# Kernel optimization log

Hardware: AMD Instinct MI355X
Metric: run time of the kernel (lower is better)

## Reference

```python
import jax, jax.numpy as jnp
import numpy as np

H = 64  # hidden_dim

def _lstm_dir(x, Wih, Whh, bih, bhh, reverse):
    # x: [B, T, D]; Wih: [4H, D]; Whh: [4H, H]; PyTorch gate order i,f,g,o
    B, T, _ = x.shape
    if reverse:
        x = x[:, ::-1, :]
    # Precompute input contribution to all gates: [B, T, 4H]
    xg = jnp.einsum('btd,gd->btg', x, Wih) + (bih + bhh)
    h0 = jnp.zeros((B, H), x.dtype)
    c0 = jnp.zeros((B, H), x.dtype)

    def step(carry, xg_t):
        h, c = carry
        g = xg_t + h @ Whh.T  # [B, 4H]
        i, f, gg, o = jnp.split(g, 4, axis=-1)
        i = jax.nn.sigmoid(i)
        f = jax.nn.sigmoid(f)
        gg = jnp.tanh(gg)
        o = jax.nn.sigmoid(o)
        c = f * c + i * gg
        h = o * jnp.tanh(c)
        return (h, c), h

    (hT, cT), hs = jax.lax.scan(step, (h0, c0), jnp.swapaxes(xg, 0, 1))
    hs = jnp.swapaxes(hs, 0, 1)  # [B, T, H]
    if reverse:
        hs = hs[:, ::-1, :]
    return hs, hT

def _forward(x, Wih_l0_f, Whh_l0_f, bih_l0_f, bhh_l0_f,
             Wih_l0_b, Whh_l0_b, bih_l0_b, bhh_l0_b,
             Wih_l1_f, Whh_l1_f, bih_l1_f, bhh_l1_f,
             Wih_l1_b, Whh_l1_b, bih_l1_b, bhh_l1_b,
             fc1_W, fc1_b, fc2_W, fc2_b):
    xt = jnp.transpose(x, (0, 2, 1))  # [B, 512, 3]
    # Layer 0 (bidirectional)
    hs_f, _ = _lstm_dir(xt, Wih_l0_f, Whh_l0_f, bih_l0_f, bhh_l0_f, False)
    hs_b, _ = _lstm_dir(xt, Wih_l0_b, Whh_l0_b, bih_l0_b, bhh_l0_b, True)
    y0 = jnp.concatenate([hs_f, hs_b], axis=-1)  # [B, 512, 2H]
    # (inter-layer dropout is identity in eval mode)
    # Layer 1 (bidirectional); only final hidden states needed
    _, hT_f = _lstm_dir(y0, Wih_l1_f, Whh_l1_f, bih_l1_f, bhh_l1_f, False)
    _, hT_b = _lstm_dir(y0, Wih_l1_b, Whh_l1_b, bih_l1_b, bhh_l1_b, True)
    h = jnp.concatenate([hT_f, hT_b], axis=-1)  # [B, 2H]
    h = jax.nn.relu(h @ fc1_W.T + fc1_b)
    return h @ fc2_W.T + fc2_b  # [B, num_classes]

def setup_inputs() -> dict:
    key = jax.random.key(0)
    ks = iter(jax.random.split(key, 32))
    B, T, C = 1024, 512, 3
    d = {}
    d['x'] = jax.random.normal(next(ks), (B, C, T), dtype=jnp.float32)
    # PyTorch-style bias init: forget-gate bias = 1, rest 0
    bias = jnp.zeros((4 * H,), jnp.float32).at[H:2 * H].set(1.0)
    for layer, din in [(0, C), (1, 2 * H)]:
        for dirn in ['f', 'b']:
            d[f'Wih_l{layer}_{dirn}'] = jax.random.normal(next(ks), (4 * H, din), dtype=jnp.float32) * 0.1
            d[f'Whh_l{layer}_{dirn}'] = jax.random.normal(next(ks), (4 * H, H), dtype=jnp.float32) * 0.1
            d[f'bih_l{layer}_{dirn}'] = bias
            d[f'bhh_l{layer}_{dirn}'] = jnp.zeros((4 * H,), jnp.float32)
    d['fc1_W'] = jax.random.normal(next(ks), (H, 2 * H), dtype=jnp.float32) * 0.1
    d['fc1_b'] = jnp.zeros((H,), jnp.float32)
    d['fc2_W'] = jax.random.normal(next(ks), (2, H), dtype=jnp.float32) * 0.1
    d['fc2_b'] = jnp.zeros((2,), jnp.float32)
    return d

def reference(x, Wih_l0_f, Whh_l0_f, bih_l0_f, bhh_l0_f,
              Wih_l0_b, Whh_l0_b, bih_l0_b, bhh_l0_b,
              Wih_l1_f, Whh_l1_f, bih_l1_f, bhh_l1_f,
              Wih_l1_b, Whh_l1_b, bih_l1_b, bhh_l1_b,
              fc1_W, fc1_b, fc2_W, fc2_b):
    return _forward(x, Wih_l0_f, Whh_l0_f, bih_l0_f, bhh_l0_f,
                    Wih_l0_b, Whh_l0_b, bih_l0_b, bhh_l0_b,
                    Wih_l1_f, Whh_l1_f, bih_l1_f, bhh_l1_f,
                    Wih_l1_b, Whh_l1_b, bih_l1_b, bhh_l1_b,
                    fc1_W, fc1_b, fc2_W, fc2_b)
```

## Files before the change

### kernel.cpp

```cpp
#include <hip/hip_runtime.h>
#include <stdint.h>

typedef __attribute__((ext_vector_type(8))) short short8;
typedef __attribute__((ext_vector_type(4))) float f32x4;

#define TT 512
#define LSTR 136
#define XS 516

static __device__ __forceinline__ uint32_t f2bf_u(float f){
  union { float f; uint32_t u; } v; v.f = f;
  return (v.u + 0x7fffu + ((v.u >> 16) & 1u)) >> 16;
}
static __device__ __forceinline__ short8 w8f32(const float* p){
  float4 a = *(const float4*)p;
  float4 b = *(const float4*)(p + 4);
  short8 r;
  r[0] = (short)f2bf_u(a.x); r[1] = (short)f2bf_u(a.y);
  r[2] = (short)f2bf_u(a.z); r[3] = (short)f2bf_u(a.w);
  r[4] = (short)f2bf_u(b.x); r[5] = (short)f2bf_u(b.y);
  r[6] = (short)f2bf_u(b.z); r[7] = (short)f2bf_u(b.w);
  return r;
}
static __device__ __forceinline__ float sigx(float x){
  float e = __builtin_amdgcn_exp2f(-1.442695040888963f * x);
  return __builtin_amdgcn_rcpf(1.f + e);
}
static __device__ __forceinline__ float tanhx(float x){
  float e = __builtin_amdgcn_exp2f(-2.885390081777927f * x);
  return fmaf(__builtin_amdgcn_rcpf(1.f + e), 2.f, -1.f);
}
static __device__ __forceinline__ void lds_barrier(){
  asm volatile("s_waitcnt lgkmcnt(0)" ::: "memory");
  __builtin_amdgcn_s_barrier();
}
#define MF(A,B,C) __builtin_amdgcn_mfma_f32_16x16x32_bf16((A),(B),(C),0,0,0)

__global__ __launch_bounds__(256, 2) void lstm_l0(
    const float* __restrict__ x,
    const float* __restrict__ Wih_f, const float* __restrict__ Whh_f,
    const float* __restrict__ bih_f, const float* __restrict__ bhh_f,
    const float* __restrict__ Wih_b, const float* __restrict__ Whh_b,
    const float* __restrict__ bih_b, const float* __restrict__ bhh_b,
    unsigned short* __restrict__ y0)
{
  const int tid = threadIdx.x;
  const int wv = tid >> 6, lane = tid & 63;
  const int quad = lane >> 4, m16 = lane & 15;
  const int dir = blockIdx.y;
  const int bbase = blockIdx.x * 4;
  const float* Wih = dir ? Wih_b : Wih_f;
  const float* Whh = dir ? Whh_b : Whh_f;
  const float* bih = dir ? bih_b : bih_f;
  const float* bhh = dir ? bhh_b : bhh_f;

  __shared__ __align__(16) unsigned short sZ[2][4][LSTR];
  __shared__ __align__(16) float sX[12 * XS];

  const int copy = m16 >> 2;
  const int batch = m16 & 3;
  const int unit = 16 * wv + 4 * copy + quad;
  const bool selA = (copy & 1) != 0;
  const bool selB = (copy & 2) != 0;

  short8 aH[4][2];
  const int gm = (m16 & 3) * 64 + (m16 >> 2);
  #pragma unroll
  for (int k = 0; k < 4; k++){
    const int g = gm + 4 * (4 * wv + k);
    aH[k][0] = w8f32(Whh + g * 64 + quad * 8);
    aH[k][1] = w8f32(Whh + g * 64 + 32 + quad * 8);
  }
  float Wf[4][3];
  f32x4 biasF;
  #pragma unroll
  for (int r = 0; r < 4; r++){
    biasF[r] = bih[r * 64 + unit] + bhh[r * 64 + unit];
    #pragma unroll
    for (int d = 0; d < 3; d++) Wf[r][d] = Wih[(r * 64 + unit) * 3 + d];
  }

  for (int idx = tid; idx < 2 * 4 * LSTR; idx += 256)
    ((unsigned short*)sZ)[idx] = 0;
  for (int i4 = tid; i4 < 1536; i4 += 256){
    const int row = i4 >> 7, t4 = (i4 & 127) * 4;
    *(float4*)&sX[row * XS + t4] = *(const float4*)(x + (size_t)bbase * 1536 + row * 512 + t4);
  }
  __syncthreads();

  const int xrow = 3 * batch;
  float c = 0.f, h = 0.f;
  const f32x4 z4 = {0.f, 0.f, 0.f, 0.f};

#define FFCOMP(F, TIDX) do { \
    float x0_ = sX[xrow * XS + (TIDX)]; \
    float x1_ = sX[(xrow + 1) * XS + (TIDX)]; \
    float x2_ = sX[(xrow + 2) * XS + (TIDX)]; \
    _Pragma("unroll") \
    for (int r_ = 0; r_ < 4; r_++) \
      F[r_] = fmaf(Wf[r_][2], x2_, fmaf(Wf[r_][1], x1_, fmaf(Wf[r_][0], x0_, biasF[r_]))); \
  } while(0)

  f32x4 FBa, FBb;
  {
    const int t0_ = dir ? (TT - 1) : 0;
    FFCOMP(FBa, t0_);
  }

#define L0STEP(S, P, FC, FN) do { \
    const int p1_ = (P) ^ 1; \
    short8 bh0 = *(const short8*)&sZ[P][batch][     quad * 8]; \
    short8 bh1 = *(const short8*)&sZ[P][batch][32 + quad * 8]; \
    if (wv == 3 && lane < 32 && (S) > 0){ \
      const int tprev = dir ? (TT - (S)) : ((S) - 1); \
      const int br_ = lane >> 3, cc_ = lane & 7; \
      uint4 v_ = *(const uint4*)&sZ[P][br_][cc_ * 8]; \
      *(uint4*)(y0 + ((size_t)(bbase + br_) * TT + tprev) * 128 + dir * 64 + cc_ * 8) = v_; \
    } \
    f32x4 C0 = MF(aH[0][0], bh0, z4); \
    f32x4 C1 = MF(aH[1][0], bh0, z4); \
    f32x4 C2 = MF(aH[2][0], bh0, z4); \
    f32x4 C3 = MF(aH[3][0], bh0, z4); \
    C0 = MF(aH[0][1], bh1, C0); \
    C1 = MF(aH[1][1], bh1, C1); \
    C2 = MF(aH[2][1], bh1, C2); \
    C3 = MF(aH[3][1], bh1, C3); \
    { int sn_ = (S) + 1; if (sn_ > TT - 1) sn_ = TT - 1; \
      const int tn_ = dir ? (TT - 1 - sn_) : sn_; \
      FFCOMP(FN, tn_); \
    } \
    __builtin_amdgcn_sched_barrier(0); \
    { \
      float g0_ = (selB ? (selA ? C3[0] : C2[0]) : (selA ? C1[0] : C0[0])) + FC[0]; \
      float g1_ = (selB ? (selA ? C3[1] : C2[1]) : (selA ? C1[1] : C0[1])) + FC[1]; \
      float g2_ = (selB ? (selA ? C3[2] : C2[2]) : (selA ? C1[2] : C0[2])) + FC[2]; \
      float g3_ = (selB ? (selA ? C3[3] : C2[3]) : (selA ? C1[3] : C0[3])) + FC[3]; \
      float ii_ = sigx(g0_), ff_ = sigx(g1_), gg_ = tanhx(g2_), oo_ = sigx(g3_); \
      c = fmaf(ff_, c, ii_ * gg_); \
      h = oo_ * tanhx(c); \
      sZ[p1_][batch][unit] = (unsigned short)f2bf_u(h); \
    } \
    __builtin_amdgcn_sched_barrier(0); \
    lds_barrier(); \
  } while(0)

  for (int s = 0; s < TT; s += 2){
    L0STEP(s,     0, FBa, FBb);
    L0STEP(s + 1, 1, FBb, FBa);
  }
#undef L0STEP
#undef FFCOMP

  if (wv == 3 && lane < 32){
    const int tl = dir ? 0 : (TT - 1);
    const int br = lane >> 3, cc = lane & 7;
    uint4 v = *(const uint4*)&sZ[0][br][cc * 8];
    *(uint4*)(y0 + ((size_t)(bbase + br) * TT + tl) * 128 + dir * 64 + cc * 8) = v;
  }
}

#define NONLIN_WRITE(A0V, A1V, P1) do { \
    float g0_ = sel0 ? (A0V)[0] : (A1V)[0]; \
    float g1_ = sel0 ? (A0V)[1] : (A1V)[1]; \
    float g2_ = sel0 ? (A0V)[2] : (A1V)[2]; \
    float g3_ = sel0 ? (A0V)[3] : (A1V)[3]; \
    float ii_ = sigx(g0_), ff_ = sigx(g1_), gg_ = tanhx(g2_), oo_ = sigx(g3_); \
    c = fmaf(ff_, c, ii_ * gg_); \
    h = oo_ * tanhx(c); \
    sZ[P1][m8][colw] = (unsigned short)f2bf_u(h); \
  } while(0)

__global__ __launch_bounds__(512, 2) void lstm_l1(
    const unsigned short* __restrict__ y0,
    const float* __restrict__ Wih_f, const float* __restrict__ Whh_f,
    const float* __restrict__ bih_f, const float* __restrict__ bhh_f,
    const float* __restrict__ Wih_b, const float* __restrict__ Whh_b,
    const float* __restrict__ bih_b, const float* __restrict__ bhh_b,
    float* __restrict__ hT)
{
  const int tid = threadIdx.x;
  const int wv = tid >> 6, lane = tid & 63;
  const int quad = lane >> 4, m16 = lane & 15;
  const int dir = blockIdx.y;
  const int bbase = blockIdx.x * 8;
  const float* Wih = dir ? Wih_b : Wih_f;
  const float* Whh = dir ? Whh_b : Whh_f;
  const float* bih = dir ? bih_b : bih_f;
  const float* bhh = dir ? bhh_b : bhh_f;

  __shared__ __align__(16) unsigned short sZ[2][8][LSTR];
  __shared__ __align__(16) unsigned short sY[4][8][LSTR];

  short8 aY[2][4], aH[2][2];
  f32x4 biasv[2];
  const int gm = (m16 & 3) * 64 + (m16 >> 2);
  #pragma unroll
  for (int i = 0; i < 2; i++){
    const int rt = 2 * wv + i;
    const int g = gm + 4 * rt;
    #pragma unroll
    for (int kt = 0; kt < 4; kt++) aY[i][kt] = w8f32(Wih + g * 128 + kt * 32 + quad * 8);
    aH[i][0] = w8f32(Whh + g * 64 + quad * 8);
    aH[i][1] = w8f32(Whh + g * 64 + 32 + quad * 8);
    const int gu = 4 * rt + quad;
    #pragma unroll
    for (int r = 0; r < 4; r++) biasv[i][r] = bih[r * 64 + gu] + bhh[r * 64 + gu];
  }

  for (int idx = tid; idx < 2 * 8 * LSTR; idx += 512)
    ((unsigned short*)sZ)[idx] = 0;

  const bool stager = (lane < 16);
  const size_t sgbase = (size_t)(bbase + wv) * TT * 128 + (size_t)lane * 8;
  float4 hA = make_float4(0.f,0.f,0.f,0.f), hB = make_float4(0.f,0.f,0.f,0.f);
  if (stager){
    const int t0 = dir ? (TT-1) : 0, t1 = dir ? (TT-2) : 1, t2 = dir ? (TT-3) : 2;
    const int t3 = dir ? (TT-4) : 3, t4 = dir ? (TT-5) : 4;
    float4 v0 = *(const float4*)(y0 + sgbase + (size_t)t0 * 128);
    float4 v1 = *(const float4*)(y0 + sgbase + (size_t)t1 * 128);
    float4 v2 = *(const float4*)(y0 + sgbase + (size_t)t2 * 128);
    hA = *(const float4*)(y0 + sgbase + (size_t)t3 * 128);
    hB = *(const float4*)(y0 + sgbase + (size_t)t4 * 128);
    *(float4*)&sY[0][wv][lane * 8] = v0;
    *(float4*)&sY[1][wv][lane * 8] = v1;
    *(float4*)&sY[2][wv][lane * 8] = v2;
  }
  __syncthreads();

  const int m8 = m16 & 7;
  const bool sel0 = (m16 < 8);
  const int colw = 8 * wv + quad + ((m16 >> 3) << 2);
  float c = 0.f, h = 0.f;

  f32x4 FBa0, FBa1, FBb0, FBb1;
  {
    short8 by0 = *(const short8*)&sY[0][m8][     quad * 8];
    short8 by1 = *(const short8*)&sY[0][m8][32 + quad * 8];
    short8 by2 = *(const short8*)&sY[0][m8][64 + quad * 8];
    short8 by3 = *(const short8*)&sY[0][m8][96 + quad * 8];
    FBa0 = MF(aY[0][0], by0, biasv[0]);
    FBa1 = MF(aY[1][0], by0, biasv[1]);
    FBa0 = MF(aY[0][1], by1, FBa0);  FBa1 = MF(aY[1][1], by1, FBa1);
    FBa0 = MF(aY[0][2], by2, FBa0);  FBa1 = MF(aY[1][2], by2, FBa1);
    FBa0 = MF(aY[0][3], by3, FBa0);  FBa1 = MF(aY[1][3], by3, FBa1);
  }

#define L1STEP(S, P, SLOT, WSLOT, HOLD, FC0, FC1, FN0, FN1) do { \
    const int p1_ = (P) ^ 1; \
    short8 bh0 = *(const short8*)&sZ[P][m8][     quad * 8]; \
    short8 bh1 = *(const short8*)&sZ[P][m8][32 + quad * 8]; \
    short8 by0 = *(const short8*)&sY[SLOT][m8][     quad * 8]; \
    short8 by1 = *(const short8*)&sY[SLOT][m8][32 + quad * 8]; \
    short8 by2 = *(const short8*)&sY[SLOT][m8][64 + quad * 8]; \
    short8 by3 = *(const short8*)&sY[SLOT][m8][96 + quad * 8]; \
    f32x4 A0 = MF(aH[0][0], bh0, FC0); \
    f32x4 A1 = MF(aH[1][0], bh0, FC1); \
    A0 = MF(aH[0][1], bh1, A0); \
    A1 = MF(aH[1][1], bh1, A1); \
    FN0 = MF(aY[0][0], by0, biasv[0]); \
    FN1 = MF(aY[1][0], by0, biasv[1]); \
    FN0 = MF(aY[0][1], by1, FN0);  FN1 = MF(aY[1][1], by1, FN1); \
    FN0 = MF(aY[0][2], by2, FN0);  FN1 = MF(aY[1][2], by2, FN1); \
    FN0 = MF(aY[0][3], by3, FN0);  FN1 = MF(aY[1][3], by3, FN1); \
    __builtin_amdgcn_sched_barrier(0); \
    NONLIN_WRITE(A0, A1, p1_); \
    if ((S) == TT - 1){ \
      hT[(size_t)(bbase + m8) * 128 + dir * 64 + colw] = h; \
    } \
    if (stager){ \
      *(float4*)&sY[WSLOT][wv][lane * 8] = HOLD; \
      int sg_ = (S) + 5; if (sg_ > TT - 1) sg_ = TT - 1; \
      const int tg_ = dir ? (TT - 1 - sg_) : sg_; \
      HOLD = *(const float4*)(y0 + sgbase + (size_t)tg_ * 128); \
    } \
    __builtin_amdgcn_sched_barrier(0); \
    lds_barrier(); \
  } while(0)

  for (int s = 0; s < TT; s += 4){
    L1STEP(s,     0, 1, 3, hA, FBa0, FBa1, FBb0, FBb1);
    L1STEP(s + 1, 1, 2, 0, hB, FBb0, FBb1, FBa0, FBa1);
    L1STEP(s + 2, 0, 3, 1, hA, FBa0, FBa1, FBb0, FBb1);
    L1STEP(s + 3, 1, 0, 2, hB, FBb0, FBb1, FBa0, FBa1);
  }
#undef L1STEP
}

__global__ __launch_bounds__(256, 1) void fc_kernel(
    const float* __restrict__ hT,
    const float* __restrict__ w1, const float* __restrict__ b1,
    const float* __restrict__ w2, const float* __restrict__ b2,
    float* __restrict__ out)
{
  __shared__ float sh[4][64];
  const int wave = threadIdx.x >> 6, lane = threadIdx.x & 63;
  const int b = blockIdx.x * 4 + wave;
  float acc = b1[lane];
  const float* hrow = hT + (size_t)b * 128;
  #pragma unroll
  for (int k = 0; k < 128; k += 4){
    float4 h4 = *(const float4*)(hrow + k);
    float4 w4 = *(const float4*)(w1 + lane * 128 + k);
    acc = fmaf(w4.x, h4.x, acc);
    acc = fmaf(w4.y, h4.y, acc);
    acc = fmaf(w4.z, h4.z, acc);
    acc = fmaf(w4.w, h4.w, acc);
  }
  sh[wave][lane] = fmaxf(acc, 0.f);
  __syncthreads();
  if (lane < 2){
    float a = b2[lane];
    #pragma unroll
    for (int k = 0; k < 64; k++) a = fmaf(w2[lane * 64 + k], sh[wave][k], a);
    out[(size_t)b * 2 + lane] = a;
  }
}

extern "C" void kernel_launch(void* const* d_in, const int* in_sizes, int n_in,
                              void* d_out, int out_size, void* d_ws, size_t ws_size,
                              hipStream_t stream){
  (void)in_sizes; (void)n_in; (void)out_size; (void)ws_size;
  const float* x     = (const float*)d_in[0];
  const float* Wih0f = (const float*)d_in[1];
  const float* Whh0f = (const float*)d_in[2];
  const float* bih0f = (const float*)d_in[3];
  const float* bhh0f = (const float*)d_in[4];
  const float* Wih0b = (const float*)d_in[5];
  const float* Whh0b = (const float*)d_in[6];
  const float* bih0b = (const float*)d_in[7];
  const float* bhh0b = (const float*)d_in[8];
  const float* Wih1f = (const float*)d_in[9];
  const float* Whh1f = (const float*)d_in[10];
  const float* bih1f = (const float*)d_in[11];
  const float* bhh1f = (const float*)d_in[12];
  const float* Wih1b = (const float*)d_in[13];
  const float* Whh1b = (const float*)d_in[14];
  const float* bih1b = (const float*)d_in[15];
  const float* bhh1b = (const float*)d_in[16];
  const float* fc1W  = (const float*)d_in[17];
  const float* fc1b  = (const float*)d_in[18];
  const float* fc2W  = (const float*)d_in[19];
  const float* fc2b  = (const float*)d_in[20];
  float* out = (float*)d_out;

  unsigned short* y0 = (unsigned short*)d_ws;
  float* hT = (float*)((char*)d_ws + (size_t)1024 * TT * 128 * 2);

  lstm_l0<<<dim3(256, 2), dim3(256), 0, stream>>>(x, Wih0f, Whh0f, bih0f, bhh0f,
                                                  Wih0b, Whh0b, bih0b, bhh0b, y0);
  lstm_l1<<<dim3(128, 2), dim3(512), 0, stream>>>(y0, Wih1f, Whh1f, bih1f, bhh1f,
                                                  Wih1b, Whh1b, bih1b, bhh1b, hT);
  fc_kernel<<<dim3(256), dim3(256), 0, stream>>>(hT, fc1W, fc1b, fc2W, fc2b, out);
}
```

Baseline: 517.1 us.

## Compute layer-1 input projection for two timesteps per MFMA batch using both half-lanes

The layer-1 kernel previously spent 8 MFMAs every step on the input projection, half of whose output lanes were discarded by the select. It now loads two consecutive timesteps' inputs into the two 8-row halves of the B operand. One 8-MFMA batch therefore yields the projections for two steps, and a ds_swizzle exchanges values between half-lanes to route each step's gates to the right lanes. The recurrent MFMAs now start from zero and the precomputed gate input is added before the nonlinearities. The staging prefetch distance grows by one slot. This halves input-projection MFMA work per step, at the cost of extra swizzles, register pressure and an alternating A/B step structure.

```diff
diff --git a/kernel.cpp b/kernel.cpp
--- a/kernel.cpp
+++ b/kernel.cpp
@@ -35,6 +35,7 @@
   __builtin_amdgcn_s_barrier();
 }
 #define MF(A,B,C) __builtin_amdgcn_mfma_f32_16x16x32_bf16((A),(B),(C),0,0,0)
+#define SWZ(x) __int_as_float(__builtin_amdgcn_ds_swizzle(__float_as_int(x), 0x201F))
 
 __global__ __launch_bounds__(256, 2) void lstm_l0(
     const float* __restrict__ x,
@@ -159,17 +160,6 @@
   }
 }
 
-#define NONLIN_WRITE(A0V, A1V, P1) do { \
-    float g0_ = sel0 ? (A0V)[0] : (A1V)[0]; \
-    float g1_ = sel0 ? (A0V)[1] : (A1V)[1]; \
-    float g2_ = sel0 ? (A0V)[2] : (A1V)[2]; \
-    float g3_ = sel0 ? (A0V)[3] : (A1V)[3]; \
-    float ii_ = sigx(g0_), ff_ = sigx(g1_), gg_ = tanhx(g2_), oo_ = sigx(g3_); \
-    c = fmaf(ff_, c, ii_ * gg_); \
-    h = oo_ * tanhx(c); \
-    sZ[P1][m8][colw] = (unsigned short)f2bf_u(h); \
-  } while(0)
-
 __global__ __launch_bounds__(512, 2) void lstm_l1(
     const unsigned short* __restrict__ y0,
     const float* __restrict__ Wih_f, const float* __restrict__ Whh_f,
@@ -214,16 +204,14 @@
   const size_t sgbase = (size_t)(bbase + wv) * TT * 128 + (size_t)lane * 8;
   float4 hA = make_float4(0.f,0.f,0.f,0.f), hB = make_float4(0.f,0.f,0.f,0.f);
   if (stager){
-    const int t0 = dir ? (TT-1) : 0, t1 = dir ? (TT-2) : 1, t2 = dir ? (TT-3) : 2;
-    const int t3 = dir ? (TT-4) : 3, t4 = dir ? (TT-5) : 4;
-    float4 v0 = *(const float4*)(y0 + sgbase + (size_t)t0 * 128);
-    float4 v1 = *(const float4*)(y0 + sgbase + (size_t)t1 * 128);
-    float4 v2 = *(const float4*)(y0 + sgbase + (size_t)t2 * 128);
-    hA = *(const float4*)(y0 + sgbase + (size_t)t3 * 128);
-    hB = *(const float4*)(y0 + sgbase + (size_t)t4 * 128);
-    *(float4*)&sY[0][wv][lane * 8] = v0;
-    *(float4*)&sY[1][wv][lane * 8] = v1;
-    *(float4*)&sY[2][wv][lane * 8] = v2;
+    #pragma unroll
+    for (int k = 0; k < 4; k++){
+      const int tk = dir ? (TT - 1 - k) : k;
+      *(float4*)&sY[k][wv][lane * 8] = *(const float4*)(y0 + sgbase + (size_t)tk * 128);
+    }
+    const int t4 = dir ? (TT - 5) : 4, t5 = dir ? (TT - 6) : 5;
+    hA = *(const float4*)(y0 + sgbase + (size_t)t4 * 128);
+    hB = *(const float4*)(y0 + sgbase + (size_t)t5 * 128);
   }
   __syncthreads();
 
@@ -231,59 +219,102 @@
   const bool sel0 = (m16 < 8);
   const int colw = 8 * wv + quad + ((m16 >> 3) << 2);
   float c = 0.f, h = 0.f;
-
-  f32x4 FBa0, FBa1, FBb0, FBb1;
-  {
-    short8 by0 = *(const short8*)&sY[0][m8][     quad * 8];
-    short8 by1 = *(const short8*)&sY[0][m8][32 + quad * 8];
-    short8 by2 = *(const short8*)&sY[0][m8][64 + quad * 8];
-    short8 by3 = *(const short8*)&sY[0][m8][96 + quad * 8];
-    FBa0 = MF(aY[0][0], by0, biasv[0]);
-    FBa1 = MF(aY[1][0], by0, biasv[1]);
-    FBa0 = MF(aY[0][1], by1, FBa0);  FBa1 = MF(aY[1][1], by1, FBa1);
-    FBa0 = MF(aY[0][2], by2, FBa0);  FBa1 = MF(aY[1][2], by2, FBa1);
-    FBa0 = MF(aY[0][3], by3, FBa0);  FBa1 = MF(aY[1][3], by3, FBa1);
-  }
-
-#define L1STEP(S, P, SLOT, WSLOT, HOLD, FC0, FC1, FN0, FN1) do { \
-    const int p1_ = (P) ^ 1; \
-    short8 bh0 = *(const short8*)&sZ[P][m8][     quad * 8]; \
-    short8 bh1 = *(const short8*)&sZ[P][m8][32 + quad * 8]; \
-    short8 by0 = *(const short8*)&sY[SLOT][m8][     quad * 8]; \
-    short8 by1 = *(const short8*)&sY[SLOT][m8][32 + quad * 8]; \
-    short8 by2 = *(const short8*)&sY[SLOT][m8][64 + quad * 8]; \
-    short8 by3 = *(const short8*)&sY[SLOT][m8][96 + quad * 8]; \
-    f32x4 A0 = MF(aH[0][0], bh0, FC0); \
-    f32x4 A1 = MF(aH[1][0], bh0, FC1); \
-    A0 = MF(aH[0][1], bh1, A0); \
-    A1 = MF(aH[1][1], bh1, A1); \
-    FN0 = MF(aY[0][0], by0, biasv[0]); \
-    FN1 = MF(aY[1][0], by0, biasv[1]); \
-    FN0 = MF(aY[0][1], by1, FN0);  FN1 = MF(aY[1][1], by1, FN1); \
-    FN0 = MF(aY[0][2], by2, FN0);  FN1 = MF(aY[1][2], by2, FN1); \
-    FN0 = MF(aY[0][3], by3, FN0);  FN1 = MF(aY[1][3], by3, FN1); \
-    __builtin_amdgcn_sched_barrier(0); \
-    NONLIN_WRITE(A0, A1, p1_); \
+  const f32x4 z4 = {0.f, 0.f, 0.f, 0.f};
+
+  const int SLOTU = 8 * LSTR;
+  const unsigned short* yb = &sY[0][0][0] + (sel0 ? 0 : SLOTU) + m8 * LSTR + quad * 8;
+
+#define FFMM(SL, FB0, FB1) do { \
+    short8 by0 = *(const short8*)(yb + (SL) * SLOTU); \
+    short8 by1 = *(const short8*)(yb + (SL) * SLOTU + 32); \
+    short8 by2 = *(const short8*)(yb + (SL) * SLOTU + 64); \
+    short8 by3 = *(const short8*)(yb + (SL) * SLOTU + 96); \
+    FB0 = MF(aY[0][0], by0, biasv[0]); \
+    FB1 = MF(aY[1][0], by0, biasv[1]); \
+    FB0 = MF(aY[0][1], by1, FB0);  FB1 = MF(aY[1][1], by1, FB1); \
+    FB0 = MF(aY[0][2], by2, FB0);  FB1 = MF(aY[1][2], by2, FB1); \
+    FB0 = MF(aY[0][3], by3, FB0);  FB1 = MF(aY[1][3], by3, FB1); \
+  } while(0)
+
+#define FFSWZ(FB0, FB1, G0, G1) do { \
+    float w10_ = SWZ(FB1[0]), w11_ = SWZ(FB1[1]), w12_ = SWZ(FB1[2]), w13_ = SWZ(FB1[3]); \
+    float w00_ = SWZ(FB0[0]), w01_ = SWZ(FB0[1]), w02_ = SWZ(FB0[2]), w03_ = SWZ(FB0[3]); \
+    G0[0] = sel0 ? FB0[0] : w10_;  G0[1] = sel0 ? FB0[1] : w11_; \
+    G0[2] = sel0 ? FB0[2] : w12_;  G0[3] = sel0 ? FB0[3] : w13_; \
+    G1[0] = sel0 ? w00_ : FB1[0];  G1[1] = sel0 ? w01_ : FB1[1]; \
+    G1[2] = sel0 ? w02_ : FB1[2];  G1[3] = sel0 ? w03_ : FB1[3]; \
+  } while(0)
+
+  f32x4 Ga0, Ga1, Gb0, Gb1, FBT0, FBT1;
+  FFMM(0, FBT0, FBT1);
+  FFSWZ(FBT0, FBT1, Ga0, Ga1);
+  lds_barrier();
+
+#define NONLIN1(R0, R1, GC, P1) do { \
+    float g0_ = (sel0 ? (R0)[0] : (R1)[0]) + GC[0]; \
+    float g1_ = (sel0 ? (R0)[1] : (R1)[1]) + GC[1]; \
+    float g2_ = (sel0 ? (R0)[2] : (R1)[2]) + GC[2]; \
+    float g3_ = (sel0 ? (R0)[3] : (R1)[3]) + GC[3]; \
+    float ii_ = sigx(g0_), ff_ = sigx(g1_), gg_ = tanhx(g2_), oo_ = sigx(g3_); \
+    c = fmaf(ff_, c, ii_ * gg_); \
+    h = oo_ * tanhx(c); \
+    sZ[P1][m8][colw] = (unsigned short)f2bf_u(h); \
+  } while(0)
+
+#define STAGE(S, WRSL, HOLD) do { \
+    if (stager){ \
+      *(float4*)&sY[WRSL][wv][lane * 8] = HOLD; \
+      int sg_ = (S) + 6; if (sg_ > TT - 1) sg_ = TT - 1; \
+      const int tg_ = dir ? (TT - 1 - sg_) : sg_; \
+      HOLD = *(const float4*)(y0 + sgbase + (size_t)tg_ * 128); \
+    } \
+  } while(0)
+
+#define L1STEPA(S, SLFF, WRSL, HOLD, GC) do { \
+    short8 bh0 = *(const short8*)&sZ[0][m8][     quad * 8]; \
+    short8 bh1 = *(const short8*)&sZ[0][m8][32 + quad * 8]; \
+    f32x4 R0 = MF(aH[0][0], bh0, z4); \
+    f32x4 R1 = MF(aH[1][0], bh0, z4); \
+    R0 = MF(aH[0][1], bh1, R0); \
+    R1 = MF(aH[1][1], bh1, R1); \
+    FFMM(SLFF, FBT0, FBT1); \
+    STAGE(S, WRSL, HOLD); \
+    __builtin_amdgcn_sched_barrier(0); \
+    NONLIN1(R0, R1, GC, 1); \
+    __builtin_amdgcn_sched_barrier(0); \
+    lds_barrier(); \
+  } while(0)
+
+#define L1STEPB(S, WRSL, HOLD, GC, GN0, GN1) do { \
+    short8 bh0 = *(const short8*)&sZ[1][m8][     quad * 8]; \
+    short8 bh1 = *(const short8*)&sZ[1][m8][32 + quad * 8]; \
+    f32x4 R0 = MF(aH[0][0], bh0, z4); \
+    f32x4 R1 = MF(aH[1][0], bh0, z4); \
+    R0 = MF(aH[0][1], bh1, R0); \
+    R1 = MF(aH[1][1], bh1, R1); \
+    FFSWZ(FBT0, FBT1, GN0, GN1); \
+    STAGE(S, WRSL, HOLD); \
+    __builtin_amdgcn_sched_barrier(0); \
+    NONLIN1(R0, R1, GC, 0); \
     if ((S) == TT - 1){ \
       hT[(size_t)(bbase + m8) * 128 + dir * 64 + colw] = h; \
     } \
-    if (stager){ \
-      *(float4*)&sY[WSLOT][wv][lane * 8] = HOLD; \
-      int sg_ = (S) + 5; if (sg_ > TT - 1) sg_ = TT - 1; \
-      const int tg_ = dir ? (TT - 1 - sg_) : sg_; \
-      HOLD = *(const float4*)(y0 + sgbase + (size_t)tg_ * 128); \
-    } \
     __builtin_amdgcn_sched_barrier(0); \
     lds_barrier(); \
   } while(0)
 
   for (int s = 0; s < TT; s += 4){
-    L1STEP(s,     0, 1, 3, hA, FBa0, FBa1, FBb0, FBb1);
-    L1STEP(s + 1, 1, 2, 0, hB, FBb0, FBb1, FBa0, FBa1);
-    L1STEP(s + 2, 0, 3, 1, hA, FBa0, FBa1, FBb0, FBb1);
-    L1STEP(s + 3, 1, 0, 2, hB, FBb0, FBb1, FBa0, FBa1);
-  }
-#undef L1STEP
+    L1STEPA(s,     2, 0, hA, Ga0);
+    L1STEPB(s + 1,    1, hB, Ga1, Gb0, Gb1);
+    L1STEPA(s + 2, 0, 2, hA, Gb0);
+    L1STEPB(s + 3,    3, hB, Gb1, Ga0, Ga1);
+  }
+#undef L1STEPA
+#undef L1STEPB
+#undef STAGE
+#undef NONLIN1
+#undef FFSWZ
+#undef FFMM
 }
 
 __global__ __launch_bounds__(256, 1) void fc_kernel(
```

After: 513.3 us. About the same (-0.7%).
